# Kernel optimization log

Hardware: AMD Instinct MI355X
Metric: run time of the kernel (lower is better)

Reference implementation:

```python
import jax, jax.numpy as jnp
import numpy as np

D_MODEL = 256
N_HEADS = 8
D_K = D_MODEL // N_HEADS
D_HID = D_MODEL // 2
LN_EPS = 1e-5


def setup_inputs() -> dict:
    key = jax.random.key(0)
    ks = jax.random.split(key, 16)
    B, ND, NT = 4, 512, 512
    s = 1.0 / np.sqrt(D_MODEL)
    inp = {
        'detections': jax.random.normal(ks[0], (B, ND, D_MODEL), jnp.float32),
        'tracks': jax.random.normal(ks[1], (B, NT, D_MODEL), jnp.float32),
        # attention projections, torch Linear convention: W [out, in], y = x W^T + b
        'w_q': jax.random.normal(ks[2], (D_MODEL, D_MODEL), jnp.float32) * s,
        'b_q': jnp.zeros((D_MODEL,), jnp.float32),
        'w_k': jax.random.normal(ks[3], (D_MODEL, D_MODEL), jnp.float32) * s,
        'b_k': jnp.zeros((D_MODEL,), jnp.float32),
        'w_v': jax.random.normal(ks[4], (D_MODEL, D_MODEL), jnp.float32) * s,
        'b_v': jnp.zeros((D_MODEL,), jnp.float32),
        'w_o': jax.random.normal(ks[5], (D_MODEL, D_MODEL), jnp.float32) * s,
        'b_o': jnp.zeros((D_MODEL,), jnp.float32),
        # LayerNorm
        'ln_g': jnp.ones((D_MODEL,), jnp.float32),
        'ln_b': jnp.zeros((D_MODEL,), jnp.float32),
        # association head MLP
        'w1': jax.random.normal(ks[6], (D_HID, D_MODEL), jnp.float32) * s,
        'b1': jnp.zeros((D_HID,), jnp.float32),
        'w2': jax.random.normal(ks[7], (1, D_HID), jnp.float32) * (1.0 / np.sqrt(D_HID)),
        'b2': jnp.zeros((1,), jnp.float32),
    }
    return inp


def _forward(detections, tracks, w_q, b_q, w_k, b_k, w_v, b_v, w_o, b_o,
             ln_g, ln_b, w1, b1, w2, b2):
    B, ND, D = detections.shape
    NT = tracks.shape[1]
    # cross-attention: query=detections, key=value=tracks
    Q = (detections @ w_q.T + b_q).reshape(B, ND, N_HEADS, D_K).transpose(0, 2, 1, 3)
    K = (tracks @ w_k.T + b_k).reshape(B, NT, N_HEADS, D_K).transpose(0, 2, 1, 3)
    V = (tracks @ w_v.T + b_v).reshape(B, NT, N_HEADS, D_K).transpose(0, 2, 1, 3)
    scores = jnp.einsum('bhqd,bhkd->bhqk', Q, K) / np.sqrt(D_K)
    attn = jax.nn.softmax(scores, axis=-1)
    ctx = jnp.einsum('bhqk,bhkd->bhqd', attn, V)  # [B,H,ND,D_K]
    ctx = ctx.transpose(0, 2, 1, 3).reshape(B, ND, D)
    attended = ctx @ w_o.T + b_o
    # residual + LayerNorm (dropout = identity in eval)
    x = detections + attended
    mu = jnp.mean(x, axis=-1, keepdims=True)
    var = jnp.var(x, axis=-1, keepdims=True)
    xn = (x - mu) * jax.lax.rsqrt(var + LN_EPS) * ln_g + ln_b
    # pairwise broadcast-multiply + 2-layer MLP + sigmoid
    combined = xn[:, :, None, :] * tracks[:, None, :, :]  # [B,ND,NT,D]
    h = jax.nn.relu(jnp.einsum('bntd,hd->bnth', combined, w1) + b1)
    logits = jnp.einsum('bnth,oh->bnto', h, w2) + b2  # [B,ND,NT,1]
    return jax.nn.sigmoid(logits[..., 0])


def reference(detections, tracks, w_q, b_q, w_k, b_k, w_v, b_v, w_o, b_o,
              ln_g, ln_b, w1, b1, w2, b2):
    return _forward(detections, tracks, w_q, b_q, w_k, b_k, w_v, b_v, w_o, b_o,
                    ln_g, ln_b, w1, b1, w2, b2)
```

## Files before the change

kernel.cpp:

```cpp
#include <hip/hip_runtime.h>

typedef _Float16 half8 __attribute__((ext_vector_type(8)));
typedef _Float16 half4v __attribute__((ext_vector_type(4)));
typedef _Float16 half2v __attribute__((ext_vector_type(2)));
typedef float f32x4 __attribute__((ext_vector_type(4)));

struct CvtJobs {
    const float* src[7];
    _Float16* dst[7];
    int n[7];
};

__global__ __launch_bounds__(256) void cvt_kernel(CvtJobs j) {
    int job = blockIdx.y;
    const float* s = j.src[job];
    _Float16* d = j.dst[job];
    int n = j.n[job];
    for (int i = blockIdx.x * blockDim.x + threadIdx.x; i < n;
         i += gridDim.x * blockDim.x)
        d[i] = (_Float16)s[i];
}

template<int MODE>
__global__ __launch_bounds__(256) void gemm_tn(
    const _Float16* __restrict__ A, const _Float16* __restrict__ Bm,
    _Float16* __restrict__ Ch, float* __restrict__ Cf,
    const float* __restrict__ bias, float alpha,
    int M, int N, int K, int lda, int ldb, int ldc)
{
    __shared__ _Float16 As[64][40];
    __shared__ _Float16 Bs[64][40];

    int tid = threadIdx.x;
    int l = tid & 63, w = tid >> 6;
    int wm = (w >> 1) * 32, wn = (w & 1) * 32;
    int m0 = blockIdx.x * 64, n0 = blockIdx.y * 64;
    int lr = tid >> 2, lc = (tid & 3) * 8;
    int ko = (l >> 4) * 8;

    f32x4 acc[2][2]{};

    for (int k0 = 0; k0 < K; k0 += 32) {
        half8 av = *(const half8*)(A + (long)(m0 + lr) * lda + k0 + lc);
        half8 bv = *(const half8*)(Bm + (long)(n0 + lr) * ldb + k0 + lc);
        __syncthreads();
        *(half8*)(&As[lr][lc]) = av;
        *(half8*)(&Bs[lr][lc]) = bv;
        __syncthreads();
        half8 a0 = *(const half8*)(&As[wm + (l & 15)][ko]);
        half8 a1 = *(const half8*)(&As[wm + 16 + (l & 15)][ko]);
        half8 b0 = *(const half8*)(&Bs[wn + (l & 15)][ko]);
        half8 b1 = *(const half8*)(&Bs[wn + 16 + (l & 15)][ko]);
        acc[0][0] = __builtin_amdgcn_mfma_f32_16x16x32_f16(a0, b0, acc[0][0], 0, 0, 0);
        acc[0][1] = __builtin_amdgcn_mfma_f32_16x16x32_f16(a0, b1, acc[0][1], 0, 0, 0);
        acc[1][0] = __builtin_amdgcn_mfma_f32_16x16x32_f16(a1, b0, acc[1][0], 0, 0, 0);
        acc[1][1] = __builtin_amdgcn_mfma_f32_16x16x32_f16(a1, b1, acc[1][1], 0, 0, 0);
    }

    #pragma unroll
    for (int mm = 0; mm < 2; ++mm)
    #pragma unroll
    for (int nn = 0; nn < 2; ++nn) {
        int row  = wm + mm * 16 + (l >> 4) * 4;
        int colg = n0 + wn + nn * 16 + (l & 15);
        float bc = bias ? bias[colg] : 0.f;
        if (MODE == 2) {
            half4v hv;
            #pragma unroll
            for (int i = 0; i < 4; ++i)
                hv[i] = (_Float16)(acc[mm][nn][i] * alpha + bc);
            int grow = m0 + row;
            int bb = grow >> 9, t = grow & 511;
            long off = ((long)(bb * 8 + (colg >> 5)) * 32 + (colg & 31)) * 512 + t;
            *(half4v*)(Ch + off) = hv;
        } else if (MODE == 0) {
            #pragma unroll
            for (int i = 0; i < 4; ++i)
                Ch[(long)(m0 + row + i) * ldc + colg] =
                    (_Float16)(acc[mm][nn][i] * alpha + bc);
        } else {
            #pragma unroll
            for (int i = 0; i < 4; ++i)
                Cf[(long)(m0 + row + i) * ldc + colg] =
                    acc[mm][nn][i] * alpha + bc;
        }
    }
}

__global__ __launch_bounds__(256) void flash_kernel(
    const _Float16* __restrict__ Q, const _Float16* __restrict__ K,
    const _Float16* __restrict__ vt, _Float16* __restrict__ ctx)
{
    __shared__ _Float16 P[4][16][264];
    int bh = blockIdx.y, b = bh >> 3, h = bh & 7;
    int q0 = blockIdx.x * 64;
    int tid = threadIdx.x, l = tid & 63, w = tid >> 6;
    int l15 = l & 15, g = l >> 4;

    const _Float16* qp = Q + ((long)b * 512 + q0 + w * 16 + l15) * 256 + h * 32 + g * 8;
    half8 qf = *(const half8*)qp;
    #pragma unroll
    for (int i = 0; i < 8; ++i) qf[i] = qf[i] * (_Float16)0.17677669529663687f;

    const _Float16* kp = K + ((long)b * 512 + l15) * 256 + h * 32 + g * 8;
    f32x4 s[32];
    f32x4 zero{};
    #pragma unroll
    for (int t = 0; t < 32; ++t) {
        half8 kf = *(const half8*)(kp + (long)t * (16 * 256));
        s[t] = __builtin_amdgcn_mfma_f32_16x16x32_f16(kf, qf, zero, 0, 0, 0);
    }
    float m0 = -3e38f, m1 = -3e38f, m2 = -3e38f, m3 = -3e38f;
    #pragma unroll
    for (int t = 0; t < 32; ++t) {
        m0 = fmaxf(m0, s[t][0]); m1 = fmaxf(m1, s[t][1]);
        m2 = fmaxf(m2, s[t][2]); m3 = fmaxf(m3, s[t][3]);
    }
    float m = fmaxf(fmaxf(m0, m1), fmaxf(m2, m3));
    m = fmaxf(m, __shfl_xor(m, 16, 64));
    m = fmaxf(m, __shfl_xor(m, 32, 64));
    float s0 = 0.f, s1 = 0.f, s2 = 0.f, s3 = 0.f;
    #pragma unroll
    for (int t = 0; t < 32; ++t) {
        s[t][0] = __expf(s[t][0] - m); s0 += s[t][0];
        s[t][1] = __expf(s[t][1] - m); s1 += s[t][1];
        s[t][2] = __expf(s[t][2] - m); s2 += s[t][2];
        s[t][3] = __expf(s[t][3] - m); s3 += s[t][3];
    }
    float sum = (s0 + s1) + (s2 + s3);
    sum += __shfl_xor(sum, 16, 64);
    sum += __shfl_xor(sum, 32, 64);
    float rs = 1.f / sum;

    f32x4 c0{}, c1{};
    const _Float16* vp = vt + ((long)bh * 32 + l15) * 512 + g * 8;
    #pragma unroll
    for (int hf = 0; hf < 2; ++hf) {
        #pragma unroll
        for (int t = 0; t < 16; ++t) {
            int tt = hf * 16 + t;
            half2v p01, p23;
            p01[0] = (_Float16)s[tt][0]; p01[1] = (_Float16)s[tt][1];
            p23[0] = (_Float16)s[tt][2]; p23[1] = (_Float16)s[tt][3];
            *(half2v*)&P[w][l15][t * 16 + g * 4]     = p01;
            *(half2v*)&P[w][l15][t * 16 + g * 4 + 2] = p23;
        }
        #pragma unroll
        for (int s2i = 0; s2i < 8; ++s2i) {
            half8 bf = *(const half8*)&P[w][l15][s2i * 32 + g * 8];
            half8 a0 = *(const half8*)(vp + hf * 256 + s2i * 32);
            half8 a1 = *(const half8*)(vp + 16 * 512 + hf * 256 + s2i * 32);
            c0 = __builtin_amdgcn_mfma_f32_16x16x32_f16(a0, bf, c0, 0, 0, 0);
            c1 = __builtin_amdgcn_mfma_f32_16x16x32_f16(a1, bf, c1, 0, 0, 0);
        }
    }
    _Float16* cp = ctx + ((long)b * 512 + q0 + w * 16 + l15) * 256 + h * 32;
    #pragma unroll
    for (int i = 0; i < 4; ++i) {
        cp[g * 4 + i]      = (_Float16)(c0[i] * rs);
        cp[16 + g * 4 + i] = (_Float16)(c1[i] * rs);
    }
}

__global__ __launch_bounds__(256) void ln_kernel(
    const float* __restrict__ det, const float* __restrict__ att,
    const float* __restrict__ g, const float* __restrict__ bta,
    _Float16* __restrict__ xn)
{
    int row = blockIdx.x, tid = threadIdx.x;
    long idx = (long)row * 256 + tid;
    float x = det[idx] + att[idx];
    float s1 = x, s2 = x * x;
    #pragma unroll
    for (int off = 32; off; off >>= 1) {
        s1 += __shfl_xor(s1, off, 64);
        s2 += __shfl_xor(s2, off, 64);
    }
    __shared__ float r1[4], r2[4];
    if ((tid & 63) == 0) { r1[tid >> 6] = s1; r2[tid >> 6] = s2; }
    __syncthreads();
    float S1 = r1[0] + r1[1] + r1[2] + r1[3];
    float S2 = r2[0] + r2[1] + r2[2] + r2[3];
    float mean = S1 * (1.f / 256.f);
    float var  = S2 * (1.f / 256.f) - mean * mean;
    float rsv = rsqrtf(var + 1e-5f);
    xn[idx] = (_Float16)((x - mean) * rsv * g[tid] + bta[tid]);
}

__global__ __launch_bounds__(256, 2) void mlp_kernel(
    const _Float16* __restrict__ xn, const _Float16* __restrict__ trk,
    const _Float16* __restrict__ w1, const float* __restrict__ w2,
    const float* __restrict__ b1, const float* __restrict__ b2,
    float* __restrict__ out)
{
    int b  = blockIdx.z;
    int n0 = blockIdx.x * 64;
    int t0 = blockIdx.y * 32;
    int tid = threadIdx.x;
    int l = tid & 63, w = tid >> 6;
    int l15 = l & 15, g = l >> 4;
    int ko = g * 8;

    __shared__ _Float16 ts[32][264];
    __shared__ float part[4][32][65];

    {
        const _Float16* src = trk + ((long)b * 512 + t0) * 256;
        int r = tid >> 3, c0 = (tid & 7) * 8;
        #pragma unroll
        for (int c = 0; c < 256; c += 64)
            *(half8*)(&ts[r][c + c0]) = *(const half8*)(src + r * 256 + c + c0);
    }

    half8 wf[2][8];
    {
        const _Float16* w1p = w1 + (w * 32 + l15) * 256 + ko;
        #pragma unroll
        for (int a = 0; a < 2; ++a)
            #pragma unroll
            for (int ks = 0; ks < 8; ++ks)
                wf[a][ks] = *(const half8*)(w1p + a * 16 * 256 + ks * 32);
    }
    f32x4 binit[2]; float w2v[2][4];
    #pragma unroll
    for (int a = 0; a < 2; ++a)
        #pragma unroll
        for (int i = 0; i < 4; ++i) {
            int hh = w * 32 + a * 16 + g * 4 + i;
            binit[a][i] = b1[hh];
            w2v[a][i]  = w2[hh];
        }

    half8 bx[4][8];
    {
        const _Float16* xb = xn + ((long)b * 512 + n0 + l15) * 256 + ko;
        #pragma unroll
        for (int mm = 0; mm < 4; ++mm)
            #pragma unroll
            for (int ks = 0; ks < 8; ++ks)
                bx[mm][ks] = *(const half8*)(xb + mm * 16 * 256 + ks * 32);
    }

    __syncthreads();

    for (int tl = 0; tl < 32; ++tl) {
        f32x4 acc[2][4];
        #pragma unroll
        for (int a = 0; a < 2; ++a)
            #pragma unroll
            for (int mm = 0; mm < 4; ++mm) acc[a][mm] = binit[a];
        #pragma unroll
        for (int ks = 0; ks < 8; ++ks) {
            half8 tf = *(const half8*)(&ts[tl][ks * 32 + ko]);
            half8 sa0 = wf[0][ks] * tf;
            half8 sa1 = wf[1][ks] * tf;
            #pragma unroll
            for (int mm = 0; mm < 4; ++mm) {
                acc[0][mm] = __builtin_amdgcn_mfma_f32_16x16x32_f16(sa0, bx[mm][ks], acc[0][mm], 0, 0, 0);
                acc[1][mm] = __builtin_amdgcn_mfma_f32_16x16x32_f16(sa1, bx[mm][ks], acc[1][mm], 0, 0, 0);
            }
        }
        #pragma unroll
        for (int mm = 0; mm < 4; ++mm) {
            float x = 0.f;
            #pragma unroll
            for (int a = 0; a < 2; ++a)
                #pragma unroll
                for (int i = 0; i < 4; ++i)
                    x = fmaf(fmaxf(acc[a][mm][i], 0.f), w2v[a][i], x);
            x += __shfl_xor(x, 16, 64);
            x += __shfl_xor(x, 32, 64);
            if (g == 0) part[w][tl][mm * 16 + l15] = x;
        }
    }
    __syncthreads();

    float b2v = b2[0];
    int t = tid & 31;
    int nbase = tid >> 5;
    float* op = out + ((long)b * 512 + n0) * 512 + t0;
    #pragma unroll
    for (int k = 0; k < 8; ++k) {
        int nn = nbase + k * 8;
        float s = part[0][t][nn] + part[1][t][nn]
                + part[2][t][nn] + part[3][t][nn] + b2v;
        op[(long)nn * 512 + t] = 1.f / (1.f + __expf(-s));
    }
}

extern "C" void kernel_launch(void* const* d_in, const int* in_sizes, int n_in,
                              void* d_out, int out_size, void* d_ws, size_t ws_size,
                              hipStream_t stream)
{
    const float* det  = (const float*)d_in[0];
    const float* trk  = (const float*)d_in[1];
    const float* w_q  = (const float*)d_in[2];
    const float* b_q  = (const float*)d_in[3];
    const float* w_k  = (const float*)d_in[4];
    const float* b_k  = (const float*)d_in[5];
    const float* w_v  = (const float*)d_in[6];
    const float* b_v  = (const float*)d_in[7];
    const float* w_o  = (const float*)d_in[8];
    const float* b_o  = (const float*)d_in[9];
    const float* ln_g = (const float*)d_in[10];
    const float* ln_b = (const float*)d_in[11];
    const float* w1   = (const float*)d_in[12];
    const float* b1   = (const float*)d_in[13];
    const float* w2   = (const float*)d_in[14];
    const float* b2   = (const float*)d_in[15];
    float* out = (float*)d_out;

    char* ws = (char*)d_ws;
    const size_t O_DETH = 0;
    const size_t O_TRKH = O_DETH + (size_t)1048576;
    const size_t O_WQH  = O_TRKH + (size_t)1048576;
    const size_t O_WKH  = O_WQH + 131072;
    const size_t O_WVH  = O_WKH + 131072;
    const size_t O_WOH  = O_WVH + 131072;
    const size_t O_W1H  = O_WOH + 131072;
    const size_t O_QH   = O_W1H + 65536;
    const size_t O_KH   = O_QH + (size_t)1048576;
    const size_t O_VT   = O_KH + (size_t)1048576;
    const size_t O_CTXH = O_VT + (size_t)1048576;
    const size_t O_XNH  = O_CTXH + (size_t)1048576;
    const size_t O_ATT  = O_XNH + (size_t)1048576;

    _Float16* det_h  = (_Float16*)(ws + O_DETH);
    _Float16* trk_h  = (_Float16*)(ws + O_TRKH);
    _Float16* wq_h   = (_Float16*)(ws + O_WQH);
    _Float16* wk_h   = (_Float16*)(ws + O_WKH);
    _Float16* wv_h   = (_Float16*)(ws + O_WVH);
    _Float16* wo_h   = (_Float16*)(ws + O_WOH);
    _Float16* w1_h   = (_Float16*)(ws + O_W1H);
    _Float16* Q_h    = (_Float16*)(ws + O_QH);
    _Float16* K_h    = (_Float16*)(ws + O_KH);
    _Float16* vt     = (_Float16*)(ws + O_VT);
    _Float16* ctx_h  = (_Float16*)(ws + O_CTXH);
    _Float16* xn_h   = (_Float16*)(ws + O_XNH);
    float*    att_f  = (float*)(ws + O_ATT);

    CvtJobs cj;
    cj.src[0] = det; cj.dst[0] = det_h; cj.n[0] = 2048 * 256;
    cj.src[1] = trk; cj.dst[1] = trk_h; cj.n[1] = 2048 * 256;
    cj.src[2] = w_q; cj.dst[2] = wq_h;  cj.n[2] = 65536;
    cj.src[3] = w_k; cj.dst[3] = wk_h;  cj.n[3] = 65536;
    cj.src[4] = w_v; cj.dst[4] = wv_h;  cj.n[4] = 65536;
    cj.src[5] = w_o; cj.dst[5] = wo_h;  cj.n[5] = 65536;
    cj.src[6] = w1;  cj.dst[6] = w1_h;  cj.n[6] = 32768;
    cvt_kernel<<<dim3(512, 7), 256, 0, stream>>>(cj);

    gemm_tn<0><<<dim3(32, 4), 256, 0, stream>>>(det_h, wq_h, Q_h, nullptr, b_q, 1.f,
        2048, 256, 256, 256, 256, 256);
    gemm_tn<0><<<dim3(32, 4), 256, 0, stream>>>(trk_h, wk_h, K_h, nullptr, b_k, 1.f,
        2048, 256, 256, 256, 256, 256);
    gemm_tn<2><<<dim3(32, 4), 256, 0, stream>>>(trk_h, wv_h, vt, nullptr, b_v, 1.f,
        2048, 256, 256, 256, 256, 256);
    flash_kernel<<<dim3(8, 32), 256, 0, stream>>>(Q_h, K_h, vt, ctx_h);
    gemm_tn<1><<<dim3(32, 4), 256, 0, stream>>>(ctx_h, wo_h, nullptr, att_f, b_o, 1.f,
        2048, 256, 256, 256, 256, 256);
    ln_kernel<<<2048, 256, 0, stream>>>(det, att_f, ln_g, ln_b, xn_h);
    mlp_kernel<<<dim3(8, 16, 4), 256, 0, stream>>>(xn_h, trk_h, w1_h, w2, b1, b2, out);

    (void)in_sizes; (void)n_in; (void)out_size; (void)ws_size;
}
```

Baseline: 195.4 us.

## Use online softmax in attention and halve MLP detection tile

The attention kernel now uses a two-chunk online softmax instead of holding all 32 score tiles in registers. This lowers register pressure at the cost of a rescale per chunk. The MLP kernel's detection tile shrinks from 64 to 32 rows per block, which doubles the grid and cuts register and shared-memory use, and its launch bound drops the min-blocks hint. The cost is that each tracks tile loaded into LDS and each set of W1 fragments now serves fewer detections.

```diff
diff --git a/kernel.cpp b/kernel.cpp
--- a/kernel.cpp
+++ b/kernel.cpp
@@ -103,45 +103,50 @@
     for (int i = 0; i < 8; ++i) qf[i] = qf[i] * (_Float16)0.17677669529663687f;
 
     const _Float16* kp = K + ((long)b * 512 + l15) * 256 + h * 32 + g * 8;
-    f32x4 s[32];
+    const _Float16* vp = vt + ((long)bh * 32 + l15) * 512 + g * 8;
+
+    f32x4 c0{}, c1{};
+    float m_run = -3e38f, sum_run = 0.f;
     f32x4 zero{};
-    #pragma unroll
-    for (int t = 0; t < 32; ++t) {
-        half8 kf = *(const half8*)(kp + (long)t * (16 * 256));
-        s[t] = __builtin_amdgcn_mfma_f32_16x16x32_f16(kf, qf, zero, 0, 0, 0);
-    }
-    float m0 = -3e38f, m1 = -3e38f, m2 = -3e38f, m3 = -3e38f;
-    #pragma unroll
-    for (int t = 0; t < 32; ++t) {
-        m0 = fmaxf(m0, s[t][0]); m1 = fmaxf(m1, s[t][1]);
-        m2 = fmaxf(m2, s[t][2]); m3 = fmaxf(m3, s[t][3]);
-    }
-    float m = fmaxf(fmaxf(m0, m1), fmaxf(m2, m3));
-    m = fmaxf(m, __shfl_xor(m, 16, 64));
-    m = fmaxf(m, __shfl_xor(m, 32, 64));
-    float s0 = 0.f, s1 = 0.f, s2 = 0.f, s3 = 0.f;
-    #pragma unroll
-    for (int t = 0; t < 32; ++t) {
-        s[t][0] = __expf(s[t][0] - m); s0 += s[t][0];
-        s[t][1] = __expf(s[t][1] - m); s1 += s[t][1];
-        s[t][2] = __expf(s[t][2] - m); s2 += s[t][2];
-        s[t][3] = __expf(s[t][3] - m); s3 += s[t][3];
-    }
-    float sum = (s0 + s1) + (s2 + s3);
-    sum += __shfl_xor(sum, 16, 64);
-    sum += __shfl_xor(sum, 32, 64);
-    float rs = 1.f / sum;
-
-    f32x4 c0{}, c1{};
-    const _Float16* vp = vt + ((long)bh * 32 + l15) * 512 + g * 8;
+
     #pragma unroll
     for (int hf = 0; hf < 2; ++hf) {
+        f32x4 s[16];
         #pragma unroll
         for (int t = 0; t < 16; ++t) {
-            int tt = hf * 16 + t;
+            half8 kf = *(const half8*)(kp + (long)(hf * 16 + t) * (16 * 256));
+            s[t] = __builtin_amdgcn_mfma_f32_16x16x32_f16(kf, qf, zero, 0, 0, 0);
+        }
+        float m0 = -3e38f, m1 = -3e38f, m2 = -3e38f, m3 = -3e38f;
+        #pragma unroll
+        for (int t = 0; t < 16; ++t) {
+            m0 = fmaxf(m0, s[t][0]); m1 = fmaxf(m1, s[t][1]);
+            m2 = fmaxf(m2, s[t][2]); m3 = fmaxf(m3, s[t][3]);
+        }
+        float ml = fmaxf(fmaxf(m0, m1), fmaxf(m2, m3));
+        ml = fmaxf(ml, __shfl_xor(ml, 16, 64));
+        ml = fmaxf(ml, __shfl_xor(ml, 32, 64));
+        float m_new = fmaxf(m_run, ml);
+        float scale = __expf(m_run - m_new);
+        #pragma unroll
+        for (int i = 0; i < 4; ++i) { c0[i] *= scale; c1[i] *= scale; }
+        sum_run *= scale;
+        float s0 = 0.f, s1 = 0.f, s2 = 0.f, s3 = 0.f;
+        #pragma unroll
+        for (int t = 0; t < 16; ++t) {
+            s[t][0] = __expf(s[t][0] - m_new); s0 += s[t][0];
+            s[t][1] = __expf(s[t][1] - m_new); s1 += s[t][1];
+            s[t][2] = __expf(s[t][2] - m_new); s2 += s[t][2];
+            s[t][3] = __expf(s[t][3] - m_new); s3 += s[t][3];
+        }
+        sum_run += (s0 + s1) + (s2 + s3);
+        m_run = m_new;
+
+        #pragma unroll
+        for (int t = 0; t < 16; ++t) {
             half2v p01, p23;
-            p01[0] = (_Float16)s[tt][0]; p01[1] = (_Float16)s[tt][1];
-            p23[0] = (_Float16)s[tt][2]; p23[1] = (_Float16)s[tt][3];
+            p01[0] = (_Float16)s[t][0]; p01[1] = (_Float16)s[t][1];
+            p23[0] = (_Float16)s[t][2]; p23[1] = (_Float16)s[t][3];
             *(half2v*)&P[w][l15][t * 16 + g * 4]     = p01;
             *(half2v*)&P[w][l15][t * 16 + g * 4 + 2] = p23;
         }
@@ -154,6 +159,9 @@
             c1 = __builtin_amdgcn_mfma_f32_16x16x32_f16(a1, bf, c1, 0, 0, 0);
         }
     }
+    sum_run += __shfl_xor(sum_run, 16, 64);
+    sum_run += __shfl_xor(sum_run, 32, 64);
+    float rs = 1.f / sum_run;
     _Float16* cp = ctx + ((long)b * 512 + q0 + w * 16 + l15) * 256 + h * 32;
     #pragma unroll
     for (int i = 0; i < 4; ++i) {
@@ -187,14 +195,14 @@
     xn[idx] = (_Float16)((x - mean) * rsv * g[tid] + bta[tid]);
 }
 
-__global__ __launch_bounds__(256, 2) void mlp_kernel(
+__global__ __launch_bounds__(256) void mlp_kernel(
     const _Float16* __restrict__ xn, const _Float16* __restrict__ trk,
     const _Float16* __restrict__ w1, const float* __restrict__ w2,
     const float* __restrict__ b1, const float* __restrict__ b2,
     float* __restrict__ out)
 {
     int b  = blockIdx.z;
-    int n0 = blockIdx.x * 64;
+    int n0 = blockIdx.x * 32;
     int t0 = blockIdx.y * 32;
     int tid = threadIdx.x;
     int l = tid & 63, w = tid >> 6;
@@ -202,14 +210,14 @@
     int ko = g * 8;
 
     __shared__ _Float16 ts[32][264];
-    __shared__ float part[4][32][65];
+    __shared__ float part[4][32][33];
 
     {
         const _Float16* src = trk + ((long)b * 512 + t0) * 256;
-        int r = tid >> 3, c0 = (tid & 7) * 8;
+        int r = tid >> 3, c0s = (tid & 7) * 8;
         #pragma unroll
         for (int c = 0; c < 256; c += 64)
-            *(half8*)(&ts[r][c + c0]) = *(const half8*)(src + r * 256 + c + c0);
+            *(half8*)(&ts[r][c + c0s]) = *(const half8*)(src + r * 256 + c + c0s);
     }
 
     half8 wf[2][8];
@@ -221,21 +229,21 @@
             for (int ks = 0; ks < 8; ++ks)
                 wf[a][ks] = *(const half8*)(w1p + a * 16 * 256 + ks * 32);
     }
-    f32x4 binit[2]; float w2v[2][4];
+    f32x4 binit[2]; f32x4 w2v[2];
     #pragma unroll
     for (int a = 0; a < 2; ++a)
         #pragma unroll
         for (int i = 0; i < 4; ++i) {
             int hh = w * 32 + a * 16 + g * 4 + i;
             binit[a][i] = b1[hh];
-            w2v[a][i]  = w2[hh];
-        }
-
-    half8 bx[4][8];
+            w2v[a][i]   = w2[hh];
+        }
+
+    half8 bx[2][8];
     {
         const _Float16* xb = xn + ((long)b * 512 + n0 + l15) * 256 + ko;
         #pragma unroll
-        for (int mm = 0; mm < 4; ++mm)
+        for (int mm = 0; mm < 2; ++mm)
             #pragma unroll
             for (int ks = 0; ks < 8; ++ks)
                 bx[mm][ks] = *(const half8*)(xb + mm * 16 * 256 + ks * 32);
@@ -244,24 +252,24 @@
     __syncthreads();
 
     for (int tl = 0; tl < 32; ++tl) {
-        f32x4 acc[2][4];
-        #pragma unroll
-        for (int a = 0; a < 2; ++a)
-            #pragma unroll
-            for (int mm = 0; mm < 4; ++mm) acc[a][mm] = binit[a];
+        f32x4 acc[2][2];
+        #pragma unroll
+        for (int a = 0; a < 2; ++a) {
+            acc[a][0] = binit[a];
+            acc[a][1] = binit[a];
+        }
         #pragma unroll
         for (int ks = 0; ks < 8; ++ks) {
             half8 tf = *(const half8*)(&ts[tl][ks * 32 + ko]);
             half8 sa0 = wf[0][ks] * tf;
             half8 sa1 = wf[1][ks] * tf;
-            #pragma unroll
-            for (int mm = 0; mm < 4; ++mm) {
-                acc[0][mm] = __builtin_amdgcn_mfma_f32_16x16x32_f16(sa0, bx[mm][ks], acc[0][mm], 0, 0, 0);
-                acc[1][mm] = __builtin_amdgcn_mfma_f32_16x16x32_f16(sa1, bx[mm][ks], acc[1][mm], 0, 0, 0);
-            }
-        }
-        #pragma unroll
-        for (int mm = 0; mm < 4; ++mm) {
+            acc[0][0] = __builtin_amdgcn_mfma_f32_16x16x32_f16(sa0, bx[0][ks], acc[0][0], 0, 0, 0);
+            acc[0][1] = __builtin_amdgcn_mfma_f32_16x16x32_f16(sa0, bx[1][ks], acc[0][1], 0, 0, 0);
+            acc[1][0] = __builtin_amdgcn_mfma_f32_16x16x32_f16(sa1, bx[0][ks], acc[1][0], 0, 0, 0);
+            acc[1][1] = __builtin_amdgcn_mfma_f32_16x16x32_f16(sa1, bx[1][ks], acc[1][1], 0, 0, 0);
+        }
+        #pragma unroll
+        for (int mm = 0; mm < 2; ++mm) {
             float x = 0.f;
             #pragma unroll
             for (int a = 0; a < 2; ++a)
@@ -280,7 +288,7 @@
     int nbase = tid >> 5;
     float* op = out + ((long)b * 512 + n0) * 512 + t0;
     #pragma unroll
-    for (int k = 0; k < 8; ++k) {
+    for (int k = 0; k < 4; ++k) {
         int nn = nbase + k * 8;
         float s = part[0][t][nn] + part[1][t][nn]
                 + part[2][t][nn] + part[3][t][nn] + b2v;
@@ -359,7 +367,7 @@
     gemm_tn<1><<<dim3(32, 4), 256, 0, stream>>>(ctx_h, wo_h, nullptr, att_f, b_o, 1.f,
         2048, 256, 256, 256, 256, 256);
     ln_kernel<<<2048, 256, 0, stream>>>(det, att_f, ln_g, ln_b, xn_h);
-    mlp_kernel<<<dim3(8, 16, 4), 256, 0, stream>>>(xn_h, trk_h, w1_h, w2, b1, b2, out);
+    mlp_kernel<<<dim3(16, 16, 4), 256, 0, stream>>>(xn_h, trk_h, w1_h, w2, b1, b2, out);
 
     (void)in_sizes; (void)n_in; (void)out_size; (void)ws_size;
 }
```

After: 201.0 us. +2.9%, slower.
